# Performance work log

Measured on AMD Instinct MI355X. Metric: run time of the kernel, lower is better.

Reference implementation:

```python
import jax, jax.numpy as jnp
import numpy as np

N_NODES = 50000
N_EDGES = 1000000
IN_DIM = 64
HID_DIM = 64
OUT_DIM = 8
N_GRAPHS = 64


def _glorot(key, shape):
    fan_in, fan_out = shape[0], shape[1]
    lim = float(np.sqrt(6.0 / (fan_in + fan_out)))
    return jax.random.uniform(key, shape, jnp.float32, -lim, lim)


def setup_inputs() -> dict:
    key = jax.random.key(0)
    ks = jax.random.split(key, 10)
    x = jax.random.normal(ks[0], (N_NODES, IN_DIM), jnp.float32)
    edge_index = jax.random.randint(ks[1], (2, N_EDGES), 0, N_NODES, jnp.int64)
    batch = jnp.sort(jax.random.randint(ks[2], (N_NODES,), 0, N_GRAPHS, jnp.int64))
    return {
        "x": x,
        "edge_index": edge_index,
        "batch": batch,
        # SAGEConv1: lin_l (applied to aggregated neighbors, has bias), lin_r (root)
        "W1_l": _glorot(ks[3], (IN_DIM, HID_DIM)),
        "b1": jnp.zeros((HID_DIM,), jnp.float32),
        "W1_r": _glorot(ks[4], (IN_DIM, HID_DIM)),
        # SAGEConv2
        "W2_l": _glorot(ks[5], (HID_DIM, HID_DIM)),
        "b2": jnp.zeros((HID_DIM,), jnp.float32),
        "W2_r": _glorot(ks[6], (HID_DIM, HID_DIM)),
        # final Linear
        "W_fc": _glorot(ks[7], (HID_DIM, OUT_DIM)),
        "b_fc": jnp.zeros((OUT_DIM,), jnp.float32),
    }


def _sage_conv(x, src, dst, W_l, b, W_r):
    # PyG SAGEConv (mean aggr): out = lin_l(mean_{j in N(i)} x_j) + lin_r(x_i)
    msg_sum = jax.ops.segment_sum(x[src], dst, num_segments=N_NODES)  # [N, d]
    deg = jax.ops.segment_sum(jnp.ones((src.shape[0],), x.dtype), dst,
                              num_segments=N_NODES)
    mean = msg_sum / jnp.maximum(deg, 1.0)[:, None]
    return mean @ W_l + b + x @ W_r


def reference(x, edge_index, batch, W1_l, b1, W1_r, W2_l, b2, W2_r, W_fc, b_fc):
    src, dst = edge_index[0], edge_index[1]
    h = jax.nn.relu(_sage_conv(x, src, dst, W1_l, b1, W1_r))
    h = jax.nn.relu(_sage_conv(h, src, dst, W2_l, b2, W2_r))
    # global_mean_pool over graph ids
    pooled_sum = jax.ops.segment_sum(h, batch, num_segments=N_GRAPHS)  # [G, d]
    counts = jax.ops.segment_sum(jnp.ones((N_NODES,), h.dtype), batch,
                                 num_segments=N_GRAPHS)
    pooled = pooled_sum / jnp.maximum(counts, 1.0)[:, None]
    return pooled @ W_fc + b_fc
```

## Files before the change

kernel.cpp:

```cpp
#include <hip/hip_runtime.h>
#include <hip/hip_bf16.h>

#define N_NODES 50000
#define N_EDGES 1000000
#define DIM 64
#define N_GRAPHS 64
#define OUT_DIM 8
#define NBLK_SCAN 196
#define NPART 8
#define SUBBLK 16
#define NODES_PER_PART (N_NODES / NPART)
#define NB_RP 512
#define CHUNK_E4 489
#define B_STRIDE 8192
#define POOL_NPW 64
#define LMPAD 80
#define XCVT_BLOCKS 3125

typedef __attribute__((ext_vector_type(8))) short short8;
typedef __attribute__((ext_vector_type(4))) float f32x4;
typedef __attribute__((ext_vector_type(4))) int v4i;

__device__ __forceinline__ unsigned short f2b(float f) {
    __hip_bfloat16 h = __float2bfloat16(f);
    return *reinterpret_cast<unsigned short*>(&h);
}
__device__ __forceinline__ float b2f(unsigned short u) {
    __hip_bfloat16 h = *reinterpret_cast<__hip_bfloat16*>(&u);
    return __bfloat162float(h);
}

__global__ void histB_kernel(const int* __restrict__ dst, int* __restrict__ blockcnt,
                             float* __restrict__ psum) {
    if (blockIdx.x == 0) {
        for (int i = threadIdx.x; i < N_GRAPHS * DIM + N_GRAPHS; i += 256)
            psum[i] = 0.0f;
    }
    __shared__ int sc[NPART];
    if (threadIdx.x < NPART) sc[threadIdx.x] = 0;
    __syncthreads();

    int e4lo = blockIdx.x * CHUNK_E4;
    int e4hi = e4lo + CHUNK_E4; if (e4hi > N_EDGES / 4) e4hi = N_EDGES / 4;

    int c0 = 0, c1 = 0, c2 = 0, c3 = 0, c4 = 0, c5 = 0, c6 = 0, c7 = 0;
    for (int e4 = e4lo + threadIdx.x; e4 < e4hi; e4 += 256) {
        v4i d = ((const v4i*)dst)[e4];
#define CNT1(DD)                                                              \
        {                                                                     \
            unsigned p = (unsigned)(DD) / NODES_PER_PART;                     \
            c0 += (p == 0); c1 += (p == 1); c2 += (p == 2); c3 += (p == 3);   \
            c4 += (p == 4); c5 += (p == 5); c6 += (p == 6); c7 += (p == 7);   \
        }
        CNT1(d.x) CNT1(d.y) CNT1(d.z) CNT1(d.w)
#undef CNT1
    }
    #pragma unroll
    for (int off = 32; off > 0; off >>= 1) {
        c0 += __shfl_xor(c0, off); c1 += __shfl_xor(c1, off);
        c2 += __shfl_xor(c2, off); c3 += __shfl_xor(c3, off);
        c4 += __shfl_xor(c4, off); c5 += __shfl_xor(c5, off);
        c6 += __shfl_xor(c6, off); c7 += __shfl_xor(c7, off);
    }
    if ((threadIdx.x & 63) == 0) {
        atomicAdd(&sc[0], c0); atomicAdd(&sc[1], c1);
        atomicAdd(&sc[2], c2); atomicAdd(&sc[3], c3);
        atomicAdd(&sc[4], c4); atomicAdd(&sc[5], c5);
        atomicAdd(&sc[6], c6); atomicAdd(&sc[7], c7);
    }
    __syncthreads();
    if (threadIdx.x < NPART) blockcnt[blockIdx.x * NPART + threadIdx.x] = sc[threadIdx.x];
}

__global__ void scan8_kernel(const int* __restrict__ blockcnt,
                             int* __restrict__ abs_off, int* __restrict__ bucket_base) {
    __shared__ int part[1024];
    int t = threadIdx.x;
    int v[4], s = 0;
    #pragma unroll
    for (int i = 0; i < 4; ++i) {
        int e = 4 * t + i;
        int p = e >> 9, b = e & (NB_RP - 1);
        v[i] = blockcnt[b * NPART + p];
        s += v[i];
    }
    part[t] = s;
    __syncthreads();
    for (int off = 1; off < 1024; off <<= 1) {
        int u = (t >= off) ? part[t - off] : 0;
        __syncthreads();
        part[t] += u;
        __syncthreads();
    }
    int base = (t == 0) ? 0 : part[t - 1];
    #pragma unroll
    for (int i = 0; i < 4; ++i) {
        int e = 4 * t + i;
        abs_off[e] = base;
        if (i == 0 && (t & 127) == 0) bucket_base[t >> 7] = base;
        base += v[i];
    }
    if (t == 1023) bucket_base[NPART] = N_EDGES;
}

__global__ void scatterP_kernel(const int* __restrict__ src, const int* __restrict__ dst,
                                const int* __restrict__ abs_off,
                                int* __restrict__ db, int* __restrict__ sb) {
    __shared__ int lcur[NPART];
    if (threadIdx.x < NPART)
        lcur[threadIdx.x] = abs_off[threadIdx.x * NB_RP + blockIdx.x];
    __syncthreads();

    int e4lo = blockIdx.x * CHUNK_E4;
    int e4hi = e4lo + CHUNK_E4; if (e4hi > N_EDGES / 4) e4hi = N_EDGES / 4;

    for (int e4 = e4lo + threadIdx.x; e4 < e4hi; e4 += 256) {
        v4i d = ((const v4i*)dst)[e4];
        v4i s = ((const v4i*)src)[e4];
#define PUT1(DD, SS)                                                          \
        {                                                                     \
            unsigned p = (unsigned)(DD) / NODES_PER_PART;                     \
            int pos = atomicAdd(&lcur[p], 1);                                 \
            db[pos] = (DD); sb[pos] = (SS);                                   \
        }
        PUT1(d.x, s.x) PUT1(d.y, s.y) PUT1(d.z, s.z) PUT1(d.w, s.w)
#undef PUT1
    }
}

__global__ void count_priv_kernel(const int* __restrict__ db,
                                  const int* __restrict__ bucket_base,
                                  int* __restrict__ privhist) {
    __shared__ int lh[NODES_PER_PART];
    int p = blockIdx.x & (NPART - 1);
    int sub = blockIdx.x >> 3;
    for (int i = threadIdx.x; i < NODES_PER_PART; i += 256) lh[i] = 0;
    __syncthreads();

    int lo = bucket_base[p], hi = bucket_base[p + 1];
    int len = hi - lo;
    int chunk = (len + SUBBLK - 1) / SUBBLK;
    int clo = lo + sub * chunk;
    int chi = clo + chunk; if (chi > hi) chi = hi;
    int nbase = p * NODES_PER_PART;

    for (int i = clo + threadIdx.x; i < chi; i += 256)
        atomicAdd(&lh[db[i] - nbase], 1);
    __syncthreads();

    int* o = privhist + (size_t)blockIdx.x * NODES_PER_PART;
    for (int i = threadIdx.x; i < NODES_PER_PART; i += 256) o[i] = lh[i];
}

__global__ void merge_hist_kernel(int* __restrict__ privhist, int* __restrict__ cnt,
                                  int* __restrict__ bsum) {
    __shared__ int sd[256];
    int t = threadIdx.x;
    int n = blockIdx.x * 256 + t;
    int run = 0;
    if (n < N_NODES) {
        int p = n / NODES_PER_PART;
        int nl = n - p * NODES_PER_PART;
        #pragma unroll
        for (int b = 0; b < SUBBLK; ++b) {
            size_t idx = (size_t)(b * NPART + p) * NODES_PER_PART + nl;
            int v = privhist[idx];
            privhist[idx] = run;
            run += v;
        }
        cnt[n] = run;
    }
    sd[t] = (n < N_NODES) ? run : 0;
    __syncthreads();
    for (int off = 128; off > 0; off >>= 1) {
        if (t < off) sd[t] += sd[t + off];
        __syncthreads();
    }
    if (t == 0) bsum[blockIdx.x] = sd[0];
}

__global__ void scan_write_kernel(const int* __restrict__ cnt, const int* __restrict__ bsum,
                                  int* __restrict__ row_start) {
    __shared__ int sb_[256];
    __shared__ int sd[256];
    __shared__ int boffs;
    int t = threadIdx.x;

    int v = (t < NBLK_SCAN) ? bsum[t] : 0;
    sb_[t] = v;
    __syncthreads();
    for (int off = 1; off < 256; off <<= 1) {
        int u = (t >= off) ? sb_[t - off] : 0;
        __syncthreads();
        sb_[t] += u;
        __syncthreads();
    }
    if (t == 0) boffs = sb_[blockIdx.x] - bsum[blockIdx.x];

    int idx = blockIdx.x * 256 + t;
    int c = (idx < N_NODES) ? cnt[idx] : 0;
    sd[t] = c;
    __syncthreads();
    for (int off = 1; off < 256; off <<= 1) {
        int u = (t >= off) ? sd[t - off] : 0;
        __syncthreads();
        sd[t] += u;
        __syncthreads();
    }
    if (idx < N_NODES) row_start[idx] = sd[t] - c + boffs;
    if (blockIdx.x == 0 && t == 0) row_start[N_NODES] = N_EDGES;
}

__global__ void fill_det_kernel(const int* __restrict__ db, const int* __restrict__ sb,
                                const int* __restrict__ bucket_base,
                                const int* __restrict__ row_start,
                                const int* __restrict__ privhist,
                                int* __restrict__ csr) {
    __shared__ int cur[NODES_PER_PART];
    int p = blockIdx.x & (NPART - 1);
    int sub = blockIdx.x >> 3;
    int nbase = p * NODES_PER_PART;
    const int* ph = privhist + (size_t)blockIdx.x * NODES_PER_PART;
    for (int i = threadIdx.x; i < NODES_PER_PART; i += 256)
        cur[i] = row_start[nbase + i] + ph[i];
    __syncthreads();

    int lo = bucket_base[p], hi = bucket_base[p + 1];
    int len = hi - lo;
    int chunk = (len + SUBBLK - 1) / SUBBLK;
    int clo = lo + sub * chunk;
    int chi = clo + chunk; if (chi > hi) chi = hi;

    for (int i = clo + threadIdx.x; i < chi; i += 256) {
        int d = db[i];
        int s = sb[i];
        int pos = atomicAdd(&cur[d - nbase], 1);
        csr[pos] = s;
    }
}

__global__ void xcvt_prep_kernel(const float* __restrict__ x, unsigned short* __restrict__ xb,
                                 const float* __restrict__ W1l, const float* __restrict__ W1r,
                                 const float* __restrict__ W2l, const float* __restrict__ W2r,
                                 unsigned short* __restrict__ Bf) {
    if (blockIdx.x < XCVT_BLOCKS) {
        int i = blockIdx.x * 256 + threadIdx.x;
        if (i >= N_NODES * DIM / 4) return;
        float4 v = ((const float4*)x)[i];
        ushort4 u;
        u.x = f2b(v.x); u.y = f2b(v.y); u.z = f2b(v.z); u.w = f2b(v.w);
        ((ushort4*)xb)[i] = u;
    } else {
        int t = (blockIdx.x - XCVT_BLOCKS) * 256 + threadIdx.x;
        if (t >= 2048) return;
        int layer = t >> 10;
        int rem = t & 1023;
        int ks = rem >> 8;
        int nt = (rem >> 6) & 3;
        int lane = rem & 63;
        int gq = lane >> 4;
        int col = nt * 16 + (lane & 15);
        const float* Wl = layer ? W2l : W1l;
        const float* Wr = layer ? W2r : W1r;
        unsigned short* o = Bf + (size_t)layer * B_STRIDE + ((ks * 4 + nt) * 64 + lane) * 8;
        #pragma unroll
        for (int i = 0; i < 8; ++i) {
            int k = ks * 32 + gq * 8 + i;
            float v = (k < DIM) ? Wl[k * DIM + col] : Wr[(k - DIM) * DIM + col];
            o[i] = f2b(v);
        }
    }
}

__global__ __launch_bounds__(256) void sage_fused_kernel(
        const unsigned short* __restrict__ feat,
        const int* __restrict__ row_start,
        const int* __restrict__ csr,
        const unsigned short* __restrict__ Bf,
        const float* __restrict__ bias,
        unsigned short* __restrict__ outb) {
    __shared__ unsigned short lmean[16][LMPAD];
    int n0 = blockIdx.x * 16;
    int wid = threadIdx.x >> 6;
    int lane = threadIdx.x & 63;
    int grp = lane >> 4;
    int fi = lane & 15;

    for (int rr = 0; rr < 4; ++rr) {
        int n = n0 + 4 * wid + rr;
        int rs = row_start[n], re = row_start[n + 1];

        float4 a0 = make_float4(0.f, 0.f, 0.f, 0.f);
        float4 a1 = make_float4(0.f, 0.f, 0.f, 0.f);
        int i = rs;
        for (; i + 8 <= re; i += 8) {
            int s0 = csr[i + grp];
            int s1 = csr[i + 4 + grp];
            ushort4 u0 = ((const ushort4*)(feat + (size_t)s0 * DIM))[fi];
            ushort4 u1 = ((const ushort4*)(feat + (size_t)s1 * DIM))[fi];
            a0.x += b2f(u0.x); a0.y += b2f(u0.y); a0.z += b2f(u0.z); a0.w += b2f(u0.w);
            a1.x += b2f(u1.x); a1.y += b2f(u1.y); a1.z += b2f(u1.z); a1.w += b2f(u1.w);
        }
        if (i + 4 <= re) {
            int s = csr[i + grp];
            ushort4 u = ((const ushort4*)(feat + (size_t)s * DIM))[fi];
            a0.x += b2f(u.x); a0.y += b2f(u.y); a0.z += b2f(u.z); a0.w += b2f(u.w);
            i += 4;
        }
        if (i + grp < re) {
            int s = csr[i + grp];
            ushort4 u = ((const ushort4*)(feat + (size_t)s * DIM))[fi];
            a1.x += b2f(u.x); a1.y += b2f(u.y); a1.z += b2f(u.z); a1.w += b2f(u.w);
        }
        float4 acc = make_float4(a0.x + a1.x, a0.y + a1.y, a0.z + a1.z, a0.w + a1.w);

        acc.x += __shfl_xor(acc.x, 16); acc.y += __shfl_xor(acc.y, 16);
        acc.z += __shfl_xor(acc.z, 16); acc.w += __shfl_xor(acc.w, 16);
        acc.x += __shfl_xor(acc.x, 32); acc.y += __shfl_xor(acc.y, 32);
        acc.z += __shfl_xor(acc.z, 32); acc.w += __shfl_xor(acc.w, 32);

        if (grp == 0) {
            float inv = 1.0f / fmaxf((float)(re - rs), 1.0f);
            ushort4 m;
            m.x = f2b(acc.x * inv); m.y = f2b(acc.y * inv);
            m.z = f2b(acc.z * inv); m.w = f2b(acc.w * inv);
            ((ushort4*)&lmean[4 * wid + rr][0])[fi] = m;
        }
    }
    __syncthreads();

    const short8* Bv = (const short8*)Bf;
    short8 bk0 = Bv[(0 * 4 + wid) * 64 + lane];
    short8 bk1 = Bv[(1 * 4 + wid) * 64 + lane];
    short8 bk2 = Bv[(2 * 4 + wid) * 64 + lane];
    short8 bk3 = Bv[(3 * 4 + wid) * 64 + lane];

    int g = lane >> 4;
    int r = lane & 15;
    f32x4 acc = {0.f, 0.f, 0.f, 0.f};

    short8 a;
    a = *(const short8*)&lmean[r][g * 8];
    acc = __builtin_amdgcn_mfma_f32_16x16x32_bf16(a, bk0, acc, 0, 0, 0);
    a = *(const short8*)&lmean[r][32 + g * 8];
    acc = __builtin_amdgcn_mfma_f32_16x16x32_bf16(a, bk1, acc, 0, 0, 0);
    const unsigned short* axp = feat + (size_t)(n0 + r) * DIM + g * 8;
    a = *(const short8*)(axp);
    acc = __builtin_amdgcn_mfma_f32_16x16x32_bf16(a, bk2, acc, 0, 0, 0);
    a = *(const short8*)(axp + 32);
    acc = __builtin_amdgcn_mfma_f32_16x16x32_bf16(a, bk3, acc, 0, 0, 0);

    float bc = bias[wid * 16 + r];
    #pragma unroll
    for (int i = 0; i < 4; ++i) {
        float v = fmaxf(acc[i] + bc, 0.0f);
        outb[(size_t)(n0 + 4 * g + i) * DIM + wid * 16 + r] = f2b(v);
    }
}

__global__ void pool_b_kernel(const unsigned short* __restrict__ h,
                              const int* __restrict__ batch,
                              float* __restrict__ psum, float* __restrict__ pcnt) {
    int wv = (blockIdx.x * blockDim.x + threadIdx.x) >> 6;
    int start = wv * POOL_NPW;
    if (start >= N_NODES) return;
    int j = threadIdx.x & 63;
    int end = start + POOL_NPW;
    if (end > N_NODES) end = N_NODES;

    int g = batch[start];
    float acc = 0.0f, cnt = 0.0f;
    for (int n = start; n < end; ++n) {
        int gn = batch[n];
        if (gn != g) {
            atomicAdd(&psum[g * DIM + j], acc);
            if (j == 0) atomicAdd(&pcnt[g], cnt);
            g = gn; acc = 0.0f; cnt = 0.0f;
        }
        acc += b2f(h[(size_t)n * DIM + j]);
        cnt += 1.0f;
    }
    atomicAdd(&psum[g * DIM + j], acc);
    if (j == 0) atomicAdd(&pcnt[g], cnt);
}

__global__ void fc_kernel(const float* __restrict__ psum,
                          const float* __restrict__ pcnt,
                          const float* __restrict__ Wfc,
                          const float* __restrict__ bfc,
                          float* __restrict__ out) {
    int tid = threadIdx.x;
    if (tid >= N_GRAPHS * OUT_DIM) return;
    int g = tid >> 3;
    int o = tid & 7;
    float inv = 1.0f / fmaxf(pcnt[g], 1.0f);
    float s = bfc[o];
    #pragma unroll
    for (int k = 0; k < DIM; ++k) {
        s += psum[g * DIM + k] * inv * Wfc[k * OUT_DIM + o];
    }
    out[g * OUT_DIM + o] = s;
}

extern "C" void kernel_launch(void* const* d_in, const int* in_sizes, int n_in,
                              void* d_out, int out_size, void* d_ws, size_t ws_size,
                              hipStream_t stream) {
    const float* x   = (const float*)d_in[0];
    const int* ei    = (const int*)d_in[1];
    const int* batch = (const int*)d_in[2];
    const float* W1l = (const float*)d_in[3];
    const float* b1  = (const float*)d_in[4];
    const float* W1r = (const float*)d_in[5];
    const float* W2l = (const float*)d_in[6];
    const float* b2  = (const float*)d_in[7];
    const float* W2r = (const float*)d_in[8];
    const float* Wfc = (const float*)d_in[9];
    const float* bfc = (const float*)d_in[10];
    float* out = (float*)d_out;

    const int* src = ei;
    const int* dst = ei + N_EDGES;

    const size_t SZ_BF   = (size_t)N_NODES * DIM * 2;
    const size_t SZ_CSR  = (size_t)N_EDGES * sizeof(int);
    const size_t SZ_CNT  = ((size_t)(N_NODES + 1) * sizeof(int) + 255) & ~(size_t)255;
    char* ws = (char*)d_ws;
    int*   csr       = (int*)(ws);
    int*   cnt       = (int*)(ws + SZ_CSR);
    int*   row_start = (int*)(ws + SZ_CSR + SZ_CNT);
    char*  tail      = ws + SZ_CSR + 2 * SZ_CNT;
    int*   bsum      = (int*)(tail);
    int*   boff      = bsum + 256;
    int*   blockcnt  = boff + 256;
    int*   abs_off   = blockcnt + NB_RP * NPART;
    int*   bucket_base = abs_off + NB_RP * NPART;
    unsigned short* Bf = (unsigned short*)(bucket_base + 16);
    float* psum      = (float*)((char*)Bf + 2 * B_STRIDE * 2);
    float* pcnt      = psum + N_GRAPHS * DIM;
    char*  regionA   = (char*)(pcnt + N_GRAPHS) + 4096;
    regionA = (char*)(((size_t)regionA + 255) & ~(size_t)255);
    int*   db        = (int*)(regionA);
    int*   sb        = (int*)(regionA + SZ_CSR);
    int*   privhist  = (int*)(regionA + 2 * SZ_CSR);
    unsigned short* xb    = (unsigned short*)(regionA);
    unsigned short* h1b   = (unsigned short*)(regionA + SZ_BF);
    unsigned short* h2b   = (unsigned short*)(regionA + 2 * SZ_BF);

    const int fusedBlocks = N_NODES / 16;
    const int poolWaves   = (N_NODES + POOL_NPW - 1) / POOL_NPW;
    const int poolBlocks  = (poolWaves + 3) / 4;

    histB_kernel<<<NB_RP, 256, 0, stream>>>(dst, blockcnt, psum);
    scan8_kernel<<<1, 1024, 0, stream>>>(blockcnt, abs_off, bucket_base);
    scatterP_kernel<<<NB_RP, 256, 0, stream>>>(src, dst, abs_off, db, sb);
    count_priv_kernel<<<NPART * SUBBLK, 256, 0, stream>>>(db, bucket_base, privhist);
    merge_hist_kernel<<<NBLK_SCAN, 256, 0, stream>>>(privhist, cnt, bsum);
    scan_write_kernel<<<NBLK_SCAN, 256, 0, stream>>>(cnt, bsum, row_start);
    fill_det_kernel<<<NPART * SUBBLK, 256, 0, stream>>>(db, sb, bucket_base, row_start,
                                                        privhist, csr);

    xcvt_prep_kernel<<<XCVT_BLOCKS + 8, 256, 0, stream>>>(x, xb, W1l, W1r, W2l, W2r, Bf);

    sage_fused_kernel<<<fusedBlocks, 256, 0, stream>>>(xb, row_start, csr, Bf, b1, h1b);
    sage_fused_kernel<<<fusedBlocks, 256, 0, stream>>>(h1b, row_start, csr,
                                                       Bf + B_STRIDE, b2, h2b);
    pool_b_kernel<<<poolBlocks, 256, 0, stream>>>(h2b, batch, psum, pcnt);
    fc_kernel<<<1, 512, 0, stream>>>(psum, pcnt, Wfc, bfc, out);
}
```

Before: 153.5 us.

## Fold scan into scatter blocks and fuse pooling with final linear

Removes the single-block scan kernel: every scatter block now redundantly rescans the 4096 block counts with 256 threads to get its own offsets, and block 0 writes the bucket bases. The atomic-based pooling and the separate FC kernel are replaced by one kernel with one block per graph. Each block binary-searches the sorted batch array for its node range, reduces in shared memory, and applies the FC layer, so psum no longer needs zeroing. This drops two launches and the global atomics, at the cost of redundant scan work in each scatter block and only 64 blocks doing the pooling.

```diff
diff --git a/kernel.cpp b/kernel.cpp
--- a/kernel.cpp
+++ b/kernel.cpp
@@ -13,7 +13,6 @@
 #define NB_RP 512
 #define CHUNK_E4 489
 #define B_STRIDE 8192
-#define POOL_NPW 64
 #define LMPAD 80
 #define XCVT_BLOCKS 3125
 
@@ -30,12 +29,7 @@
     return __bfloat162float(h);
 }
 
-__global__ void histB_kernel(const int* __restrict__ dst, int* __restrict__ blockcnt,
-                             float* __restrict__ psum) {
-    if (blockIdx.x == 0) {
-        for (int i = threadIdx.x; i < N_GRAPHS * DIM + N_GRAPHS; i += 256)
-            psum[i] = 0.0f;
-    }
+__global__ void histB_kernel(const int* __restrict__ dst, int* __restrict__ blockcnt) {
     __shared__ int sc[NPART];
     if (threadIdx.x < NPART) sc[threadIdx.x] = 0;
     __syncthreads();
@@ -72,21 +66,26 @@
     if (threadIdx.x < NPART) blockcnt[blockIdx.x * NPART + threadIdx.x] = sc[threadIdx.x];
 }
 
-__global__ void scan8_kernel(const int* __restrict__ blockcnt,
-                             int* __restrict__ abs_off, int* __restrict__ bucket_base) {
-    __shared__ int part[1024];
+__global__ void scatterP_kernel(const int* __restrict__ src, const int* __restrict__ dst,
+                                const int* __restrict__ blockcnt,
+                                int* __restrict__ db, int* __restrict__ sb,
+                                int* __restrict__ bucket_base) {
+    __shared__ int part[256];
+    __shared__ int lcur[NPART];
     int t = threadIdx.x;
-    int v[4], s = 0;
+    int bid = blockIdx.x;
+
+    int v[16], s = 0;
     #pragma unroll
-    for (int i = 0; i < 4; ++i) {
-        int e = 4 * t + i;
+    for (int i = 0; i < 16; ++i) {
+        int e = 16 * t + i;
         int p = e >> 9, b = e & (NB_RP - 1);
         v[i] = blockcnt[b * NPART + p];
         s += v[i];
     }
     part[t] = s;
     __syncthreads();
-    for (int off = 1; off < 1024; off <<= 1) {
+    for (int off = 1; off < 256; off <<= 1) {
         int u = (t >= off) ? part[t - off] : 0;
         __syncthreads();
         part[t] += u;
@@ -94,36 +93,28 @@
     }
     int base = (t == 0) ? 0 : part[t - 1];
     #pragma unroll
-    for (int i = 0; i < 4; ++i) {
-        int e = 4 * t + i;
-        abs_off[e] = base;
-        if (i == 0 && (t & 127) == 0) bucket_base[t >> 7] = base;
+    for (int i = 0; i < 16; ++i) {
+        int e = 16 * t + i;
+        if ((e & (NB_RP - 1)) == bid) lcur[e >> 9] = base;
+        if (bid == 0 && (e & (NB_RP - 1)) == 0) bucket_base[e >> 9] = base;
         base += v[i];
     }
-    if (t == 1023) bucket_base[NPART] = N_EDGES;
-}
-
-__global__ void scatterP_kernel(const int* __restrict__ src, const int* __restrict__ dst,
-                                const int* __restrict__ abs_off,
-                                int* __restrict__ db, int* __restrict__ sb) {
-    __shared__ int lcur[NPART];
-    if (threadIdx.x < NPART)
-        lcur[threadIdx.x] = abs_off[threadIdx.x * NB_RP + blockIdx.x];
-    __syncthreads();
-
-    int e4lo = blockIdx.x * CHUNK_E4;
+    if (bid == 0 && t == 0) bucket_base[NPART] = N_EDGES;
+    __syncthreads();
+
+    int e4lo = bid * CHUNK_E4;
     int e4hi = e4lo + CHUNK_E4; if (e4hi > N_EDGES / 4) e4hi = N_EDGES / 4;
 
-    for (int e4 = e4lo + threadIdx.x; e4 < e4hi; e4 += 256) {
+    for (int e4 = e4lo + t; e4 < e4hi; e4 += 256) {
         v4i d = ((const v4i*)dst)[e4];
-        v4i s = ((const v4i*)src)[e4];
+        v4i s4 = ((const v4i*)src)[e4];
 #define PUT1(DD, SS)                                                          \
         {                                                                     \
             unsigned p = (unsigned)(DD) / NODES_PER_PART;                     \
             int pos = atomicAdd(&lcur[p], 1);                                 \
             db[pos] = (DD); sb[pos] = (SS);                                   \
         }
-        PUT1(d.x, s.x) PUT1(d.y, s.y) PUT1(d.z, s.z) PUT1(d.w, s.w)
+        PUT1(d.x, s4.x) PUT1(d.y, s4.y) PUT1(d.z, s4.z) PUT1(d.w, s4.w)
 #undef PUT1
     }
 }
@@ -358,48 +349,40 @@
     }
 }
 
-__global__ void pool_b_kernel(const unsigned short* __restrict__ h,
-                              const int* __restrict__ batch,
-                              float* __restrict__ psum, float* __restrict__ pcnt) {
-    int wv = (blockIdx.x * blockDim.x + threadIdx.x) >> 6;
-    int start = wv * POOL_NPW;
-    if (start >= N_NODES) return;
-    int j = threadIdx.x & 63;
-    int end = start + POOL_NPW;
-    if (end > N_NODES) end = N_NODES;
-
-    int g = batch[start];
-    float acc = 0.0f, cnt = 0.0f;
-    for (int n = start; n < end; ++n) {
-        int gn = batch[n];
-        if (gn != g) {
-            atomicAdd(&psum[g * DIM + j], acc);
-            if (j == 0) atomicAdd(&pcnt[g], cnt);
-            g = gn; acc = 0.0f; cnt = 0.0f;
-        }
+__global__ void pool_fc_kernel(const unsigned short* __restrict__ h,
+                               const int* __restrict__ batch,
+                               const float* __restrict__ Wfc,
+                               const float* __restrict__ bfc,
+                               float* __restrict__ out) {
+    __shared__ float cs[4][DIM];
+    __shared__ float colsum[DIM];
+    int g = blockIdx.x;
+    int tid = threadIdx.x;
+    int wid = tid >> 6, j = tid & 63;
+
+    int lo = 0, hi = N_NODES;
+    while (lo < hi) { int m = (lo + hi) >> 1; if (batch[m] < g) lo = m + 1; else hi = m; }
+    int glo = lo;
+    lo = 0; hi = N_NODES;
+    while (lo < hi) { int m = (lo + hi) >> 1; if (batch[m] < g + 1) lo = m + 1; else hi = m; }
+    int ghi = lo;
+
+    float acc = 0.0f;
+    for (int n = glo + wid; n < ghi; n += 4)
         acc += b2f(h[(size_t)n * DIM + j]);
-        cnt += 1.0f;
-    }
-    atomicAdd(&psum[g * DIM + j], acc);
-    if (j == 0) atomicAdd(&pcnt[g], cnt);
-}
-
-__global__ void fc_kernel(const float* __restrict__ psum,
-                          const float* __restrict__ pcnt,
-                          const float* __restrict__ Wfc,
-                          const float* __restrict__ bfc,
-                          float* __restrict__ out) {
-    int tid = threadIdx.x;
-    if (tid >= N_GRAPHS * OUT_DIM) return;
-    int g = tid >> 3;
-    int o = tid & 7;
-    float inv = 1.0f / fmaxf(pcnt[g], 1.0f);
-    float s = bfc[o];
-    #pragma unroll
-    for (int k = 0; k < DIM; ++k) {
-        s += psum[g * DIM + k] * inv * Wfc[k * OUT_DIM + o];
-    }
-    out[g * OUT_DIM + o] = s;
+    cs[wid][j] = acc;
+    __syncthreads();
+    if (wid == 0) colsum[j] = cs[0][j] + cs[1][j] + cs[2][j] + cs[3][j];
+    __syncthreads();
+
+    if (tid < OUT_DIM) {
+        float inv = 1.0f / fmaxf((float)(ghi - glo), 1.0f);
+        float s = bfc[tid];
+        #pragma unroll
+        for (int k = 0; k < DIM; ++k)
+            s += colsum[k] * inv * Wfc[k * OUT_DIM + tid];
+        out[g * OUT_DIM + tid] = s;
+    }
 }
 
 extern "C" void kernel_launch(void* const* d_in, const int* in_sizes, int n_in,
@@ -447,12 +430,9 @@
     unsigned short* h2b   = (unsigned short*)(regionA + 2 * SZ_BF);
 
     const int fusedBlocks = N_NODES / 16;
-    const int poolWaves   = (N_NODES + POOL_NPW - 1) / POOL_NPW;
-    const int poolBlocks  = (poolWaves + 3) / 4;
-
-    histB_kernel<<<NB_RP, 256, 0, stream>>>(dst, blockcnt, psum);
-    scan8_kernel<<<1, 1024, 0, stream>>>(blockcnt, abs_off, bucket_base);
-    scatterP_kernel<<<NB_RP, 256, 0, stream>>>(src, dst, abs_off, db, sb);
+
+    histB_kernel<<<NB_RP, 256, 0, stream>>>(dst, blockcnt);
+    scatterP_kernel<<<NB_RP, 256, 0, stream>>>(src, dst, blockcnt, db, sb, bucket_base);
     count_priv_kernel<<<NPART * SUBBLK, 256, 0, stream>>>(db, bucket_base, privhist);
     merge_hist_kernel<<<NBLK_SCAN, 256, 0, stream>>>(privhist, cnt, bsum);
     scan_write_kernel<<<NBLK_SCAN, 256, 0, stream>>>(cnt, bsum, row_start);
@@ -464,6 +444,5 @@
     sage_fused_kernel<<<fusedBlocks, 256, 0, stream>>>(xb, row_start, csr, Bf, b1, h1b);
     sage_fused_kernel<<<fusedBlocks, 256, 0, stream>>>(h1b, row_start, csr,
                                                        Bf + B_STRIDE, b2, h2b);
-    pool_b_kernel<<<poolBlocks, 256, 0, stream>>>(h2b, batch, psum, pcnt);
-    fc_kernel<<<1, 512, 0, stream>>>(psum, pcnt, Wfc, bfc, out);
-}
+    pool_fc_kernel<<<N_GRAPHS, 256, 0, stream>>>(h2b, batch, Wfc, bfc, out);
+}
```

After: 178.5 us. +16.2%, slower.
